# Performance work log

Hardware: AMD Instinct MI355X
Metric: run time of the kernel (lower is better)

The kernel has to match this reference:

```python
import jax, jax.numpy as jnp
import numpy as np

D_MODEL = 1024
NUM_HEADS = 16
DEPTH = D_MODEL // NUM_HEADS
BATCH = 2
SEQ = 2048


def setup_inputs() -> dict:
    key = jax.random.key(0)
    ks = jax.random.split(key, 12)
    s = 1.0 / np.sqrt(D_MODEL)
    inp = {
        'v': jax.random.normal(ks[0], (BATCH, SEQ, D_MODEL), jnp.float32),
        'k': jax.random.normal(ks[1], (BATCH, SEQ, D_MODEL), jnp.float32),
        'q': jax.random.normal(ks[2], (BATCH, SEQ, D_MODEL), jnp.float32),
        # causal mask: 1.0 where attention is disallowed (strict upper triangle)
        'mask': jnp.triu(jnp.ones((1, 1, SEQ, SEQ), jnp.float32), k=1),
        'Wq': jax.random.normal(ks[3], (D_MODEL, D_MODEL), jnp.float32) * s,
        'bq': jnp.zeros((D_MODEL,), jnp.float32),
        'Wk': jax.random.normal(ks[4], (D_MODEL, D_MODEL), jnp.float32) * s,
        'bk': jnp.zeros((D_MODEL,), jnp.float32),
        'Wv': jax.random.normal(ks[5], (D_MODEL, D_MODEL), jnp.float32) * s,
        'bv': jnp.zeros((D_MODEL,), jnp.float32),
        'Wo': jax.random.normal(ks[6], (D_MODEL, D_MODEL), jnp.float32) * s,
        'bo': jnp.zeros((D_MODEL,), jnp.float32),
    }
    return inp


def _split_heads(x):
    b, s, _ = x.shape
    return x.reshape(b, s, NUM_HEADS, DEPTH).transpose(0, 2, 1, 3)  # [B,H,S,Dh]


def reference(v, k, q, mask, Wq, bq, Wk, bk, Wv, bv, Wo, bo):
    b = q.shape[0]
    qh = _split_heads(q @ Wq.T + bq)
    kh = _split_heads(k @ Wk.T + bk)
    vh = _split_heads(v @ Wv.T + bv)
    scores = jnp.einsum('bhsd,bhtd->bhst', qh, kh) / jnp.sqrt(
        jnp.asarray(DEPTH, jnp.float32))
    scores = scores + mask * (-1e9)
    attn = jax.nn.softmax(scores, axis=-1)
    out = jnp.einsum('bhst,bhtd->bhsd', attn, vh)
    out = out.transpose(0, 2, 1, 3).reshape(b, -1, D_MODEL)
    return out @ Wo.T + bo
```

## Files before the change

### kernel.cpp

```cpp
#include <hip/hip_runtime.h>
#include <hip/hip_bf16.h>

#define D_MODEL 1024
#define NHEADS 16
#define DEPTH 64
#define BATCH 2
#define SEQ 2048
#define NTOK (BATCH * SEQ)

#define QSCALE 0.180336884f
#define DEFER_THR 11.5415603f

typedef short bf16x8 __attribute__((ext_vector_type(8)));
typedef float f32x4 __attribute__((ext_vector_type(4)));
typedef float f32x16 __attribute__((ext_vector_type(16)));
typedef unsigned short ushortx8 __attribute__((ext_vector_type(8)));
typedef unsigned uint2v __attribute__((ext_vector_type(2)));

using gas_ptr = const __attribute__((address_space(1))) unsigned int*;
using las_ptr = __attribute__((address_space(3))) unsigned int*;

__device__ __forceinline__ unsigned short f2bf(float f) {
    union { float f; unsigned u; } v; v.f = f;
    unsigned r = v.u + 0x7fffu + ((v.u >> 16) & 1u);
    return (unsigned short)(r >> 16);
}

__device__ __forceinline__ unsigned cvtpk(float lo, float hi) {
    unsigned r;
    asm("v_cvt_pk_bf16_f32 %0, %1, %2" : "=v"(r) : "v"(lo), "v"(hi));
    return r;
}

__device__ __forceinline__ uint2v pls(unsigned a, unsigned b) {
    return __builtin_amdgcn_permlane32_swap(a, b, false, false);
}

__device__ __forceinline__ void gload16(const void* g, void* l) {
    __builtin_amdgcn_global_load_lds((gas_ptr)g, (las_ptr)l, 16, 0, 0);
}

__global__ __launch_bounds__(256) void convert_bf16(
    const float* __restrict__ q, const float* __restrict__ k, const float* __restrict__ v,
    const float* __restrict__ wq, const float* __restrict__ wk,
    const float* __restrict__ wv, const float* __restrict__ wo,
    unsigned short* __restrict__ qb, unsigned short* __restrict__ kb,
    unsigned short* __restrict__ vb,
    unsigned short* __restrict__ wqb, unsigned short* __restrict__ wkb,
    unsigned short* __restrict__ wvb, unsigned short* __restrict__ wob)
{
    const int ACT = (NTOK * D_MODEL) / 8;
    const int WT  = (D_MODEL * D_MODEL) / 8;
    const int total = 3 * ACT + 4 * WT;
    for (int i = blockIdx.x * 256 + threadIdx.x; i < total; i += gridDim.x * 256) {
        const float* s; unsigned short* d; int off; float sc = 1.f;
        if (i < ACT)            { s = q; d = qb; off = i; }
        else if (i < 2 * ACT)   { s = k; d = kb; off = i - ACT; }
        else if (i < 3 * ACT)   { s = v; d = vb; off = i - 2 * ACT; }
        else {
            int j = i - 3 * ACT;
            int wsel = j >> 17;  off = j & (WT - 1);
            s = (wsel == 0) ? wq : (wsel == 1) ? wk : (wsel == 2) ? wv : wo;
            d = (wsel == 0) ? wqb : (wsel == 1) ? wkb : (wsel == 2) ? wvb : wob;
            if (wsel == 0) sc = QSCALE;
        }
        float4 a = ((const float4*)s)[off * 2];
        float4 b = ((const float4*)s)[off * 2 + 1];
        ushortx8 r;
        r[0] = f2bf(a.x * sc); r[1] = f2bf(a.y * sc);
        r[2] = f2bf(a.z * sc); r[3] = f2bf(a.w * sc);
        r[4] = f2bf(b.x * sc); r[5] = f2bf(b.y * sc);
        r[6] = f2bf(b.z * sc); r[7] = f2bf(b.w * sc);
        ((ushortx8*)d)[off] = r;
    }
}

template<int IT, int DEST, bool QKV>
__global__ __launch_bounds__(256) void gemm_bf16(
    const unsigned short* __restrict__ A0, const unsigned short* __restrict__ A1,
    const unsigned short* __restrict__ A2,
    const unsigned short* __restrict__ B0, const unsigned short* __restrict__ B1,
    const unsigned short* __restrict__ B2,
    const float* __restrict__ bias0, const float* __restrict__ bias1,
    const float* __restrict__ bias2,
    void* __restrict__ C0, void* __restrict__ C1, void* __restrict__ C2,
    int M, int N, int K)
{
    constexpr int BM = IT * 32;
    constexpr int WROWS = IT * 16;
    __shared__ unsigned short As[BM * 64];
    __shared__ unsigned short Bs[128 * 64];

    const unsigned short* A = A0; const unsigned short* Bw = B0;
    const float* bias = bias0;    void* Cp = C0;
    float bsc = 1.f;
    int zz = 0;
    if (QKV) {
        zz = blockIdx.z;
        if (zz == 0) bsc = QSCALE;
        if (zz == 1) { A = A1; Bw = B1; bias = bias1; Cp = C1; }
        else if (zz == 2) { A = A2; Bw = B2; bias = bias2; Cp = C2; }
    }

    const int tid  = threadIdx.x;
    const int lane = tid & 63;
    const int w    = tid >> 6;
    const int wu   = __builtin_amdgcn_readfirstlane(w);
    const int wr   = w >> 1, wc = w & 1;
    const int lr   = lane & 15, lg = lane >> 4;

    const int row0 = blockIdx.y * BM;
    const int n0   = blockIdx.x * 128;

    const int srow = lane >> 3, scol = (lane & 7) * 8;
    const unsigned short* gA[IT];
    for (int c = 0; c < IT; ++c)
        gA[c] = A + (size_t)(row0 + (c * 4 + wu) * 8 + srow) * K + scol;
    const unsigned short* gB[4];
    for (int c = 0; c < 4; ++c)
        gB[c] = Bw + (size_t)(n0 + (c * 4 + wu) * 8 + srow) * K + scol;

    f32x4 acc[IT][4];
    for (int i = 0; i < IT; ++i)
        for (int j = 0; j < 4; ++j)
            for (int r = 0; r < 4; ++r) acc[i][j][r] = 0.f;

    for (int kt = 0; kt < K; kt += 64) {
        for (int c = 0; c < IT; ++c)
            gload16(gA[c] + kt, &As[(c * 4 + wu) * 512]);
        for (int c = 0; c < 4; ++c)
            gload16(gB[c] + kt, &Bs[(c * 4 + wu) * 512]);
        __syncthreads();

        bf16x8 af[IT][2], bfr[4][2];
        for (int i = 0; i < IT; ++i)
            for (int kk = 0; kk < 2; ++kk)
                af[i][kk] = *(const bf16x8*)&As[(wr * WROWS + i * 16 + lr) * 64 + kk * 32 + lg * 8];
        for (int j = 0; j < 4; ++j)
            for (int kk = 0; kk < 2; ++kk)
                bfr[j][kk] = *(const bf16x8*)&Bs[(wc * 64 + j * 16 + lr) * 64 + kk * 32 + lg * 8];
        for (int kk = 0; kk < 2; ++kk)
            for (int i = 0; i < IT; ++i)
                for (int j = 0; j < 4; ++j)
                    acc[i][j] = __builtin_amdgcn_mfma_f32_16x16x32_bf16(
                        af[i][kk], bfr[j][kk], acc[i][j], 0, 0, 0);
        __syncthreads();
    }

    for (int i = 0; i < IT; ++i) {
        for (int j = 0; j < 4; ++j) {
            int gcol = n0 + wc * 64 + j * 16 + lr;
            float bv = bias[gcol] * bsc;
            int s0full = row0 + wr * WROWS + i * 16 + lg * 4;
            if (QKV && zz == 1) {
                int b_ = s0full >> 11, sr = s0full & (SEQ - 1);
                int h_ = gcol >> 6, dh = gcol & 63;
                int jt_ = sr >> 6, t0 = sr & 63;
                int tb_ = t0 >> 5, m0 = t0 & 31;
                int dk_ = dh >> 4, hi_ = (dh >> 3) & 1, e_ = dh & 7;
                unsigned short* Kf = (unsigned short*)Cp;
                size_t base = ((size_t)(b_ * NHEADS + h_) * (SEQ >> 6) + jt_) * 4096
                            + (size_t)((tb_ * 4 + dk_) * 64 + hi_ * 32) * 8 + e_;
#pragma unroll
                for (int r = 0; r < 4; ++r)
                    Kf[base + (size_t)(m0 + r) * 8] = f2bf(acc[i][j][r] + bv);
            } else if (QKV && zz == 2) {
                int b_ = s0full >> 11, sr = s0full & (SEQ - 1);
                int h_ = gcol >> 6, dh = gcol & 63;
                int jt_ = sr >> 6, t0 = sr & 63;
                int ts_ = t0 >> 4, hi_ = (t0 >> 3) & 1, e0 = t0 & 7;
                int dblk = dh >> 5, m_ = dh & 31;
                unsigned w0 = (unsigned)f2bf(acc[i][j][0] + bv)
                            | ((unsigned)f2bf(acc[i][j][1] + bv) << 16);
                unsigned w1 = (unsigned)f2bf(acc[i][j][2] + bv)
                            | ((unsigned)f2bf(acc[i][j][3] + bv) << 16);
                unsigned long long pk = (unsigned long long)w0
                                      | ((unsigned long long)w1 << 32);
                unsigned short* Vf = (unsigned short*)Cp;
                size_t idx = ((size_t)(b_ * NHEADS + h_) * (SEQ >> 6) + jt_) * 4096
                           + (size_t)((dblk * 4 + ts_) * 64 + hi_ * 32 + m_) * 8 + e0;
                *(unsigned long long*)&Vf[idx] = pk;
            } else if (DEST == 0) {
#pragma unroll
                for (int r = 0; r < 4; ++r) {
                    int grow = s0full + r;
                    float val = acc[i][j][r] + bv;
                    int b_ = grow >> 11, s = grow & (SEQ - 1);
                    int h_ = gcol >> 6, dh = gcol & 63;
                    ((unsigned short*)Cp)[(((size_t)b_ * NHEADS + h_) * SEQ + s) * DEPTH + dh]
                        = f2bf(val);
                }
            } else {
#pragma unroll
                for (int r = 0; r < 4; ++r) {
                    int grow = s0full + r;
                    ((float*)Cp)[(size_t)grow * N + gcol] = acc[i][j][r] + bv;
                }
            }
        }
    }
}

#define KLOAD(JT, KF)                                                          \
{                                                                              \
    const unsigned short* Kt_ = Kb + (size_t)(JT) * 4096;                      \
    _Pragma("unroll")                                                          \
    for (int f_ = 0; f_ < 8; ++f_)                                             \
        KF[f_] = *(const bf16x8*)&Kt_[(size_t)f_ * 512 + lane * 8];            \
}

#define TILE_BODY(KC, KN)                                                      \
{                                                                              \
    const unsigned short* Vg = Vb + (size_t)jt * 4096;                         \
    bf16x8 vf0[4], vf1[4];                                                     \
    _Pragma("unroll")                                                          \
    for (int ts = 0; ts < 4; ++ts) {                                           \
        vf0[ts] = *(const bf16x8*)&Vg[(size_t)ts * 512 + lane * 8];            \
        vf1[ts] = *(const bf16x8*)&Vg[(size_t)(4 + ts) * 512 + lane * 8];      \
    }                                                                          \
    if (jt + 2 < ntiles) { KLOAD(jt + 2, KN) }                                 \
    f32x16 st[2];                                                              \
    __builtin_amdgcn_s_setprio(1);                                             \
    _Pragma("unroll")                                                          \
    for (int tb = 0; tb < 2; ++tb) {                                           \
        f32x16 a;                                                              \
        _Pragma("unroll") for (int r = 0; r < 16; ++r) a[r] = 0.f;             \
        _Pragma("unroll")                                                      \
        for (int dk = 0; dk < 4; ++dk)                                         \
            a = __builtin_amdgcn_mfma_f32_32x32x16_bf16(KC[tb * 4 + dk], qf[dk], a, 0, 0, 0); \
        st[tb] = a;                                                            \
    }                                                                          \
    __builtin_amdgcn_s_setprio(0);                                             \
    if (jt == ntiles - 1) {                                                    \
        _Pragma("unroll")                                                      \
        for (int tb = 0; tb < 2; ++tb)                                         \
            _Pragma("unroll")                                                  \
            for (int r = 0; r < 16; ++r) {                                     \
                int t = jt * 64 + tb * 32 + (r & 3) + 8 * (r >> 2) + 4 * hi;   \
                if (t > qr0 + m) st[tb][r] = -1e9f;                            \
            }                                                                  \
    }                                                                          \
    float tmx[16];                                                             \
    _Pragma("unroll")                                                          \
    for (int r = 0; r < 16; ++r) tmx[r] = fmaxf(st[0][r], st[1][r]);           \
    _Pragma("unroll")                                                          \
    for (int sft = 8; sft; sft >>= 1)                                          \
        _Pragma("unroll")                                                      \
        for (int r = 0; r < 8; ++r)                                            \
            if (r < sft) tmx[r] = fmaxf(tmx[r], tmx[r + sft]);                 \
    float tmax;                                                                \
    {                                                                          \
        union { float f; unsigned u; } cu_; cu_.f = tmx[0];                    \
        uint2v rr_ = pls(cu_.u, cu_.u);                                        \
        union { unsigned u; float f; } a_, b_; a_.u = rr_[0]; b_.u = rr_[1];   \
        tmax = fmaxf(a_.f, b_.f);                                              \
    }                                                                          \
    if (!__all(tmax <= mrun + DEFER_THR)) {                                    \
        float mnew = fmaxf(mrun, tmax);                                        \
        float sc = exp2f(mrun - mnew);                                         \
        mrun = mnew; lrun *= sc;                                               \
        if (hi == 0) scbw[m] = sc;                                             \
        f32x4 s4[4];                                                           \
        _Pragma("unroll")                                                      \
        for (int g = 0; g < 4; ++g) s4[g] = *(f32x4*)&scbw[g * 8 + hi * 4];    \
        _Pragma("unroll")                                                      \
        for (int r = 0; r < 16; ++r) {                                         \
            float f = s4[r >> 2][r & 3];                                       \
            o0[r] *= f; o1[r] *= f;                                            \
        }                                                                      \
    }                                                                          \
    float psum = 0.f;                                                          \
    _Pragma("unroll")                                                          \
    for (int tb = 0; tb < 2; ++tb)                                             \
        _Pragma("unroll")                                                      \
        for (int r = 0; r < 16; ++r) {                                         \
            float p = exp2f(st[tb][r] - mrun);                                 \
            st[tb][r] = p; psum += p;                                          \
        }                                                                      \
    {                                                                          \
        union { float f; unsigned u; } cu_; cu_.f = psum;                      \
        uint2v rr_ = pls(cu_.u, cu_.u);                                        \
        union { unsigned u; float f; } a_, b_; a_.u = rr_[0]; b_.u = rr_[1];   \
        lrun += a_.f + b_.f;                                                   \
    }                                                                          \
    unsigned pkw[8][2];                                                        \
    _Pragma("unroll")                                                          \
    for (int G = 0; G < 8; ++G) {                                              \
        const int tb = G >> 2, g = G & 3;                                      \
        pkw[G][0] = cvtpk(st[tb][4 * g + 0], st[tb][4 * g + 1]);               \
        pkw[G][1] = cvtpk(st[tb][4 * g + 2], st[tb][4 * g + 3]);               \
    }                                                                          \
    __builtin_amdgcn_s_setprio(1);                                             \
    _Pragma("unroll")                                                          \
    for (int ts = 0; ts < 4; ++ts) {                                           \
        uint2v s0_ = pls(pkw[2 * ts][0], pkw[2 * ts + 1][0]);                  \
        uint2v s1_ = pls(pkw[2 * ts][1], pkw[2 * ts + 1][1]);                  \
        union { unsigned u[4]; bf16x8 v; } uu;                                 \
        uu.u[0] = s0_[0]; uu.u[1] = s1_[0]; uu.u[2] = s0_[1]; uu.u[3] = s1_[1]; \
        o0 = __builtin_amdgcn_mfma_f32_32x32x16_bf16(uu.v, vf0[ts], o0, 0, 0, 0); \
        o1 = __builtin_amdgcn_mfma_f32_32x32x16_bf16(uu.v, vf1[ts], o1, 0, 0, 0); \
    }                                                                          \
    __builtin_amdgcn_s_setprio(0);                                             \
}

__global__ __launch_bounds__(128, 2) void attn_wave(
    const unsigned short* __restrict__ Qh, const unsigned short* __restrict__ Kh,
    const unsigned short* __restrict__ Vt, unsigned short* __restrict__ ctx)
{
    __shared__ __align__(16) float scb[2][32];
    __shared__ __align__(16) float mlbuf[2][2][32];
    __shared__ __align__(16) float c0b[32], c1b[32], invb[32];
    __shared__ __align__(16) float osh0[16][64], osh1[16][64];

    const int tid  = threadIdx.x;
    const int ww   = tid >> 6;
    const int lane = tid & 63;
    const int m    = lane & 31;
    const int hi   = lane >> 5;
    float* scbw = scb[ww];

    const int bid  = blockIdx.x;
    const int bh   = bid & 31;
    const int qb   = 63 - (bid >> 5);
    const int qr0  = qb * 32;

    const int b = bh >> 4, h = bh & 15;
    const unsigned short* Qb = Qh + ((size_t)bh * SEQ + qr0) * DEPTH;
    const unsigned short* Kb = Kh + (size_t)bh * SEQ * DEPTH;
    const unsigned short* Vb = Vt + (size_t)bh * SEQ * DEPTH;

    bf16x8 qf[4];
#pragma unroll
    for (int dk = 0; dk < 4; ++dk)
        qf[dk] = *(const bf16x8*)&Qb[(size_t)m * DEPTH + dk * 16 + hi * 8];

    f32x16 o0, o1;
#pragma unroll
    for (int r = 0; r < 16; ++r) { o0[r] = 0.f; o1[r] = 0.f; }
    float mrun = -1e30f, lrun = 0.f;

    const int ntiles = (qb >> 1) + 1;
    bf16x8 kfA[8], kfB[8];

    int jt = ww;
    if (jt < ntiles) {
        KLOAD(jt, kfA)
        while (true) {
            TILE_BODY(kfA, kfB)
            jt += 2; if (jt >= ntiles) break;
            TILE_BODY(kfB, kfA)
            jt += 2; if (jt >= ntiles) break;
        }
    }

    if (hi == 0) { mlbuf[ww][0][m] = mrun; mlbuf[ww][1][m] = lrun; }
    __syncthreads();
    if (ww == 0 && hi == 0) {
        float m0 = mlbuf[0][0][m], l0 = mlbuf[0][1][m];
        float m1 = mlbuf[1][0][m], l1 = mlbuf[1][1][m];
        float M  = fmaxf(m0, m1);
        float c0 = exp2f(m0 - M), c1 = exp2f(m1 - M);
        c0b[m] = c0; c1b[m] = c1;
        invb[m] = 1.0f / (l0 * c0 + l1 * c1);
    }
    __syncthreads();

    const float* cb = (ww == 0) ? c0b : c1b;
    f32x4 fc[4];
#pragma unroll
    for (int g = 0; g < 4; ++g)
        fc[g] = *(const f32x4*)&cb[g * 8 + hi * 4];
#pragma unroll
    for (int r = 0; r < 16; ++r) {
        float f = fc[r >> 2][r & 3];
        o0[r] *= f; o1[r] *= f;
    }
    if (ww == 0) {
#pragma unroll
        for (int r = 0; r < 16; ++r) { osh0[r][lane] = o0[r]; osh1[r][lane] = o1[r]; }
    }
    __syncthreads();
    if (ww == 1) {
        f32x4 fi[4];
#pragma unroll
        for (int g = 0; g < 4; ++g)
            fi[g] = *(const f32x4*)&invb[g * 8 + hi * 4];
#pragma unroll
        for (int r = 0; r < 16; ++r) {
            float inv = fi[r >> 2][r & 3];
            int ml = (r & 3) + 8 * (r >> 2) + 4 * hi;
            size_t rowbase = ((size_t)b * SEQ + qr0 + ml) * D_MODEL + h * DEPTH;
            ctx[rowbase + m]      = f2bf((o0[r] + osh0[r][lane]) * inv);
            ctx[rowbase + 32 + m] = f2bf((o1[r] + osh1[r][lane]) * inv);
        }
    }
}

extern "C" void kernel_launch(void* const* d_in, const int* in_sizes, int n_in,
                              void* d_out, int out_size, void* d_ws, size_t ws_size,
                              hipStream_t stream) {
    const float* v  = (const float*)d_in[0];
    const float* k  = (const float*)d_in[1];
    const float* q  = (const float*)d_in[2];
    const float* Wq = (const float*)d_in[4];
    const float* bq = (const float*)d_in[5];
    const float* Wk = (const float*)d_in[6];
    const float* bk = (const float*)d_in[7];
    const float* Wv = (const float*)d_in[8];
    const float* bv = (const float*)d_in[9];
    const float* Wo = (const float*)d_in[10];
    const float* bo = (const float*)d_in[11];

    char* ws = (char*)d_ws;
    const size_t MB = 1024 * 1024;
    unsigned short* Qb  = (unsigned short*)(ws + 0);
    unsigned short* Kb  = (unsigned short*)(ws + 8  * MB);
    unsigned short* Vb  = (unsigned short*)(ws + 16 * MB);
    unsigned short* Wqb = (unsigned short*)(ws + 24 * MB);
    unsigned short* Wkb = (unsigned short*)(ws + 26 * MB);
    unsigned short* Wvb = (unsigned short*)(ws + 28 * MB);
    unsigned short* Wob = (unsigned short*)(ws + 30 * MB);
    unsigned short* Qh  = (unsigned short*)(ws + 32 * MB);
    unsigned short* Kh  = (unsigned short*)(ws + 40 * MB);
    unsigned short* Vtt = (unsigned short*)(ws + 48 * MB);
    unsigned short* ctx = Qb;

    convert_bf16<<<2048, 256, 0, stream>>>(q, k, v, Wq, Wk, Wv, Wo,
                                           Qb, Kb, Vb, Wqb, Wkb, Wvb, Wob);

    gemm_bf16<4, 0, true><<<dim3(8, 32, 3), 256, 0, stream>>>(
        Qb, Kb, Vb, Wqb, Wkb, Wvb, bq, bk, bv,
        (void*)Qh, (void*)Kh, (void*)Vtt, NTOK, D_MODEL, D_MODEL);

    attn_wave<<<dim3(2048), 128, 0, stream>>>(Qh, Kh, Vtt, ctx);

    gemm_bf16<2, 1, false><<<dim3(8, 64), 256, 0, stream>>>(
        ctx, nullptr, nullptr, Wob, nullptr, nullptr, bo, nullptr, nullptr,
        d_out, nullptr, nullptr, NTOK, D_MODEL, D_MODEL);
}
```

Baseline: 121.7 us.

## Double-buffer GEMM LDS tiles with K-step 32 to overlap loads and MFMA

Restructures the bf16 GEMM main loop to use two LDS buffers with a K-tile of 32, issuing the next tile's global-to-LDS loads before computing on the current tile. One barrier per iteration replaces the previous two, and global load latency is meant to overlap with MFMA work. The cost is twice as many loop iterations with half the MFMA work each, which means more barriers in total and a different global access pattern (64-byte row segments instead of 128).

```diff
diff --git a/kernel.cpp b/kernel.cpp
--- a/kernel.cpp
+++ b/kernel.cpp
@@ -88,8 +88,8 @@
 {
     constexpr int BM = IT * 32;
     constexpr int WROWS = IT * 16;
-    __shared__ unsigned short As[BM * 64];
-    __shared__ unsigned short Bs[128 * 64];
+    __shared__ unsigned short As[2][BM * 32];
+    __shared__ unsigned short Bs[2][128 * 32];
 
     const unsigned short* A = A0; const unsigned short* Bw = B0;
     const float* bias = bias0;    void* Cp = C0;
@@ -112,39 +112,56 @@
     const int row0 = blockIdx.y * BM;
     const int n0   = blockIdx.x * 128;
 
-    const int srow = lane >> 3, scol = (lane & 7) * 8;
-    const unsigned short* gA[IT];
-    for (int c = 0; c < IT; ++c)
-        gA[c] = A + (size_t)(row0 + (c * 4 + wu) * 8 + srow) * K + scol;
-    const unsigned short* gB[4];
-    for (int c = 0; c < 4; ++c)
-        gB[c] = Bw + (size_t)(n0 + (c * 4 + wu) * 8 + srow) * K + scol;
+    const int cA0 = wu * 64 + lane;
+    const unsigned short* gA0 = A + (size_t)(row0 + (cA0 >> 2)) * K + (cA0 & 3) * 8;
+    const unsigned short* gA1 = nullptr;
+    if (IT == 4) {
+        const int cA1 = 256 + cA0;
+        gA1 = A + (size_t)(row0 + (cA1 >> 2)) * K + (cA1 & 3) * 8;
+    }
+    const unsigned short* gB0 = Bw + (size_t)(n0 + (cA0 >> 2)) * K + (cA0 & 3) * 8;
+    const unsigned short* gB1;
+    {
+        const int cB1 = 256 + cA0;
+        gB1 = Bw + (size_t)(n0 + (cB1 >> 2)) * K + (cB1 & 3) * 8;
+    }
+
+    auto STAGE = [&](int kt, int buf) {
+        gload16(gA0 + kt, &As[buf][wu * 512]);
+        if (IT == 4) gload16(gA1 + kt, &As[buf][2048 + wu * 512]);
+        gload16(gB0 + kt, &Bs[buf][wu * 512]);
+        gload16(gB1 + kt, &Bs[buf][2048 + wu * 512]);
+    };
 
     f32x4 acc[IT][4];
     for (int i = 0; i < IT; ++i)
         for (int j = 0; j < 4; ++j)
             for (int r = 0; r < 4; ++r) acc[i][j][r] = 0.f;
 
-    for (int kt = 0; kt < K; kt += 64) {
-        for (int c = 0; c < IT; ++c)
-            gload16(gA[c] + kt, &As[(c * 4 + wu) * 512]);
-        for (int c = 0; c < 4; ++c)
-            gload16(gB[c] + kt, &Bs[(c * 4 + wu) * 512]);
+    STAGE(0, 0);
+    __syncthreads();
+
+    const int NT = K / 32;
+    int cur = 0;
+    for (int t = 0; t < NT; ++t) {
+        if (t + 1 < NT) STAGE((t + 1) * 32, cur ^ 1);
+
+        bf16x8 af[IT], bfr[4];
+#pragma unroll
+        for (int i = 0; i < IT; ++i)
+            af[i] = *(const bf16x8*)&As[cur][(wr * WROWS + i * 16 + lr) * 32 + lg * 8];
+#pragma unroll
+        for (int j = 0; j < 4; ++j)
+            bfr[j] = *(const bf16x8*)&Bs[cur][(wc * 64 + j * 16 + lr) * 32 + lg * 8];
+#pragma unroll
+        for (int i = 0; i < IT; ++i)
+#pragma unroll
+            for (int j = 0; j < 4; ++j)
+                acc[i][j] = __builtin_amdgcn_mfma_f32_16x16x32_bf16(
+                    af[i], bfr[j], acc[i][j], 0, 0, 0);
+
         __syncthreads();
-
-        bf16x8 af[IT][2], bfr[4][2];
-        for (int i = 0; i < IT; ++i)
-            for (int kk = 0; kk < 2; ++kk)
-                af[i][kk] = *(const bf16x8*)&As[(wr * WROWS + i * 16 + lr) * 64 + kk * 32 + lg * 8];
-        for (int j = 0; j < 4; ++j)
-            for (int kk = 0; kk < 2; ++kk)
-                bfr[j][kk] = *(const bf16x8*)&Bs[(wc * 64 + j * 16 + lr) * 64 + kk * 32 + lg * 8];
-        for (int kk = 0; kk < 2; ++kk)
-            for (int i = 0; i < IT; ++i)
-                for (int j = 0; j < 4; ++j)
-                    acc[i][j] = __builtin_amdgcn_mfma_f32_16x16x32_bf16(
-                        af[i][kk], bfr[j][kk], acc[i][j], 0, 0, 0);
-        __syncthreads();
+        cur ^= 1;
     }
 
     for (int i = 0; i < IT; ++i) {
```

Result: faster. 118.5 us (-2.6%).
